# Kernel tuning notes

Measured on AMD Instinct MI355X. Metric: run time of the kernel, lower is better.

Reference implementation:

```python
import jax, jax.numpy as jnp
import numpy as np

N, D, K = 65536, 512, 512


def _l2norm(x, eps=1e-12):
    # matches torch F.normalize: x / max(||x||, eps)
    n = jnp.linalg.norm(x, axis=-1, keepdims=True)
    return x / jnp.maximum(n, eps)


def setup_inputs() -> dict:
    key = jax.random.key(0)
    k1, k2 = jax.random.split(key)
    return {
        "embeddings": jax.random.normal(k1, (N, D), dtype=jnp.float32),
        "labels": jax.random.randint(k2, (N,), 0, K),
        "w": jnp.asarray(10.0, dtype=jnp.float32),
        "b": jnp.asarray(-5.0, dtype=jnp.float32),
        "num_classes": K,
    }


def reference(embeddings, labels, w, b, num_classes):
    # assumes labels take all values in [0, num_classes) so torch.unique's
    # inverse == labels (holds for the generated inputs: 65536 draws over 512 ids)
    labels = labels.astype(jnp.int32)
    n = embeddings.shape[0]
    emb = _l2norm(embeddings)                                        # [N, D]
    ones = jnp.ones((n,), dtype=emb.dtype)
    counts = jax.ops.segment_sum(ones, labels, num_segments=num_classes)   # [K]
    sums = jax.ops.segment_sum(emb, labels, num_segments=num_classes)      # [K, D]
    centroids = sums / jnp.maximum(counts, 1.0)[:, None]             # [K, D] (NOT re-normalized, per source)
    sims = emb @ centroids.T                                          # [N, K]
    # exclusive centroid for each sample's own class, vectorized over N
    cnt_i = counts[labels]                                            # [N]
    denom = jnp.maximum(cnt_i - 1.0, 1.0)[:, None]
    excl = _l2norm((sums[labels] - emb) / denom)                      # [N, D]
    own = jnp.sum(emb * excl, axis=-1)                                # [N]
    rows = jnp.arange(n)
    cur = sims[rows, labels]
    own = jnp.where(cnt_i > 1.0, own, cur)                            # skip singleton classes
    sims = sims.at[rows, labels].set(own)
    logits = jnp.maximum(w, 1e-6) * sims + b
    logp = jax.nn.log_softmax(logits, axis=-1)
    return -jnp.mean(logp[rows, labels])
```

## Files before the change

kernel.cpp:

```cpp
#include <hip/hip_runtime.h>
#include <hip/hip_bf16.h>

#define N_ROWS 65536
#define DIM    512
#define KCLS   512
#define BUCKET 256

typedef __bf16 bf16x8 __attribute__((ext_vector_type(8)));
typedef float  f32x16 __attribute__((ext_vector_type(16)));

__device__ __forceinline__ float bf2f(ushort u) {
    union { unsigned int i; float f; } v; v.i = ((unsigned int)u) << 16; return v.f;
}

__global__ __launch_bounds__(256) void rnorm_embb_kernel(
    const float* __restrict__ emb, const int* __restrict__ labels,
    ushort* __restrict__ embb, int* __restrict__ counts,
    ushort* __restrict__ order16)
{
    const int tid  = threadIdx.x;
    const int wave = tid >> 6;
    const int lane = tid & 63;
    const int row  = blockIdx.x * 4 + wave;

    const float4* ep = (const float4*)(emb + (size_t)row * DIM + lane * 8);
    const float4 e0 = ep[0], e1 = ep[1];
    float ss = e0.x*e0.x + e0.y*e0.y + e0.z*e0.z + e0.w*e0.w
             + e1.x*e1.x + e1.y*e1.y + e1.z*e1.z + e1.w*e1.w;
    #pragma unroll
    for (int off = 1; off < 64; off <<= 1)
        ss += __shfl_xor(ss, off, 64);
    const float rn = 1.0f / fmaxf(sqrtf(ss), 1e-12f);

    bf16x8 h;
    h[0] = (__bf16)(e0.x * rn); h[1] = (__bf16)(e0.y * rn);
    h[2] = (__bf16)(e0.z * rn); h[3] = (__bf16)(e0.w * rn);
    h[4] = (__bf16)(e1.x * rn); h[5] = (__bf16)(e1.y * rn);
    h[6] = (__bf16)(e1.z * rn); h[7] = (__bf16)(e1.w * rn);
    *(bf16x8*)(embb + (size_t)row * DIM + lane * 8) = h;

    if (lane == 0) {
        const int l   = labels[row];
        const int pos = atomicAdd(&counts[l], 1);
        order16[l * BUCKET + pos] = (ushort)row;
    }
}

__global__ __launch_bounds__(256) void class_sum_kernel(
    const ushort* __restrict__ embb,
    const int* __restrict__ counts, const ushort* __restrict__ order16,
    float* __restrict__ sums, ushort* __restrict__ centb)
{
    __shared__ float part[4][DIM];

    const int cls  = blockIdx.x;
    const int tid  = threadIdx.x;
    const int wave = tid >> 6;
    const int lane = tid & 63;
    const int cnt  = counts[cls];
    const int base = cls * BUCKET;
    const int d8   = lane * 8;

    float a[8] = {};
    float b2[8] = {};
    int j = wave;
    for (; j + 4 < cnt; j += 8) {
        const int r1 = order16[base + j];
        const int r2 = order16[base + j + 4];
        const uint4 u1 = *(const uint4*)(embb + (size_t)r1 * DIM + d8);
        const uint4 u2 = *(const uint4*)(embb + (size_t)r2 * DIM + d8);
        const ushort* s1 = (const ushort*)&u1;
        const ushort* s2 = (const ushort*)&u2;
        #pragma unroll
        for (int q = 0; q < 8; ++q) { a[q] += bf2f(s1[q]); b2[q] += bf2f(s2[q]); }
    }
    if (j < cnt) {
        const int r = order16[base + j];
        const uint4 u = *(const uint4*)(embb + (size_t)r * DIM + d8);
        const ushort* s1 = (const ushort*)&u;
        #pragma unroll
        for (int q = 0; q < 8; ++q) a[q] += bf2f(s1[q]);
    }
    #pragma unroll
    for (int q = 0; q < 8; ++q) part[wave][d8 + q] = a[q] + b2[q];
    __syncthreads();

    const int d0 = tid * 2;
    const float s0 = part[0][d0]   + part[1][d0]   + part[2][d0]   + part[3][d0];
    const float s1 = part[0][d0+1] + part[1][d0+1] + part[2][d0+1] + part[3][d0+1];
    *(float2*)(sums + (size_t)cls * DIM + d0) = make_float2(s0, s1);
    const float cinv = 1.0f / fmaxf((float)cnt, 1.0f);
    const __bf16 c0 = (__bf16)(s0 * cinv);
    const __bf16 c1 = (__bf16)(s1 * cinv);
    ushort2 cpk;
    cpk.x = *(const ushort*)&c0;
    cpk.y = *(const ushort*)&c1;
    *(ushort2*)(centb + (size_t)cls * DIM + d0) = cpk;
}

#define A_STRIDE 40
#define B_STRIDE 40
__global__ __launch_bounds__(256, 3) void fused_loss_kernel(
    const ushort* __restrict__ embb, const int* __restrict__ labels,
    const int* __restrict__ counts, const float* __restrict__ sums,
    const ushort* __restrict__ centb,
    const float* __restrict__ wp, const float* __restrict__ bp,
    float* __restrict__ loss_acc, int* __restrict__ done,
    float* __restrict__ out)
{
    __shared__ __align__(16) ushort A_lds[64 * A_STRIDE];
    __shared__ __align__(16) ushort B_lds[256 * B_STRIDE];
    __shared__ float m_part[4][64];
    __shared__ float s_part[4][64];
    __shared__ float ll_s[64];
    __shared__ float own_s[64];
    __shared__ int   lbl_s[64];
    __shared__ int   rep_s[64];

    const int tid  = threadIdx.x;
    const int wave = tid >> 6;
    const int lane = tid & 63;
    const int ln31 = lane & 31;
    const int half = lane >> 5;
    const int r0   = blockIdx.x * 64;

    m_part[wave][lane] = -1e30f;
    s_part[wave][lane] = 0.f;

    for (int rr = wave; rr < 64; rr += 4) {
        const int row = r0 + rr;
        const int l   = labels[row];
        const uint4 ev = *(const uint4*)(embb + (size_t)row * DIM + lane * 8);
        const ushort* eu = (const ushort*)&ev;
        const float4* sp = (const float4*)(sums + (size_t)l * DIM + lane * 8);
        const float4 s0 = sp[0], s1 = sp[1];
        const float sv[8] = {s0.x, s0.y, s0.z, s0.w, s1.x, s1.y, s1.z, s1.w};
        float d1 = 0.f, d2 = 0.f;
        #pragma unroll
        for (int jj = 0; jj < 8; ++jj) {
            const float e  = bf2f(eu[jj]);
            const float df = sv[jj] - e;
            d1 += e * df;
            d2 += df * df;
        }
        #pragma unroll
        for (int off = 32; off > 0; off >>= 1) {
            d1 += __shfl_down(d1, off, 64);
            d2 += __shfl_down(d2, off, 64);
        }
        if (lane == 0) {
            own_s[rr] = d1 / fmaxf(sqrtf(d2), 1e-12f);
            lbl_s[rr] = l;
            rep_s[rr] = (counts[l] > 1) ? 1 : 0;
        }
    }
    __syncthreads();

    const int srow = tid >> 2;
    const int sch  = (tid & 3) * 8;
    const ushort* aSrc = embb + (size_t)(r0 + srow) * DIM + sch;
    ushort* aDst = A_lds + srow * A_STRIDE + sch;
    ushort* bDst = B_lds + srow * B_STRIDE + sch;
    const ushort* Ard = A_lds + ln31 * A_STRIDE + half * 8;
    const ushort* Brd = B_lds + (wave * 64 + ln31) * B_STRIDE + half * 8;

    const int rot = (blockIdx.x * 7) & 15;
    const float wv = fmaxf(wp[0], 1e-6f);
    const float bv = bp[0];

    #pragma unroll 1
    for (int ph = 0; ph < 2; ++ph) {
        const ushort* bBase = centb + (size_t)(ph * 256) * DIM;
        f32x16 acc[2][2] = {};

        #pragma unroll 1
        for (int ic = 0; ic < 16; ++ic) {
            const int kk = ((ic + rot) & 15) * 32;
            *(uint4*)aDst = *(const uint4*)(aSrc + kk);
            #pragma unroll
            for (int it = 0; it < 4; ++it)
                *(uint4*)(bDst + it * 64 * B_STRIDE) =
                    *(const uint4*)(bBase + (size_t)(srow + it * 64) * DIM + sch + kk);
            __syncthreads();

            #pragma unroll
            for (int ks = 0; ks < 2; ++ks) {
                const int ko = ks * 16;
                const bf16x8 a0 = *(const bf16x8*)(Ard + ko);
                const bf16x8 a1 = *(const bf16x8*)(Ard + 32 * A_STRIDE + ko);
                const bf16x8 b0 = *(const bf16x8*)(Brd + ko);
                const bf16x8 b1 = *(const bf16x8*)(Brd + 32 * B_STRIDE + ko);
                acc[0][0] = __builtin_amdgcn_mfma_f32_32x32x16_bf16(a0, b0, acc[0][0], 0, 0, 0);
                acc[0][1] = __builtin_amdgcn_mfma_f32_32x32x16_bf16(a0, b1, acc[0][1], 0, 0, 0);
                acc[1][0] = __builtin_amdgcn_mfma_f32_32x32x16_bf16(a1, b0, acc[1][0], 0, 0, 0);
                acc[1][1] = __builtin_amdgcn_mfma_f32_32x32x16_bf16(a1, b1, acc[1][1], 0, 0, 0);
            }
            __syncthreads();
        }

        #pragma unroll
        for (int mt = 0; mt < 2; ++mt) {
            #pragma unroll
            for (int reg = 0; reg < 16; ++reg) {
                const int row = mt * 32 + (reg & 3) + 8 * (reg >> 2) + 4 * half;
                const int lbl = lbl_s[row];
                float vals[2];
                float mx = -1e30f;
                #pragma unroll
                for (int jn = 0; jn < 2; ++jn) {
                    const int col = ph * 256 + wave * 64 + jn * 32 + ln31;
                    float lg = wv * acc[mt][jn][reg] + bv;
                    if (col == lbl) {
                        if (rep_s[row]) lg = wv * own_s[row] + bv;
                        ll_s[row] = lg;
                    }
                    vals[jn] = lg;
                    mx = fmaxf(mx, lg);
                }
                #pragma unroll
                for (int off = 1; off < 32; off <<= 1)
                    mx = fmaxf(mx, __shfl_xor(mx, off, 64));
                float s = __expf(vals[0] - mx) + __expf(vals[1] - mx);
                #pragma unroll
                for (int off = 1; off < 32; off <<= 1)
                    s += __shfl_xor(s, off, 64);
                if (ln31 == 0) {
                    const float mo = m_part[wave][row];
                    const float mn = fmaxf(mo, mx);
                    s_part[wave][row] = s_part[wave][row] * __expf(mo - mn)
                                      + s * __expf(mx - mn);
                    m_part[wave][row] = mn;
                }
            }
        }
    }
    __syncthreads();

    if (tid < 64) {
        const int row = tid;
        float m0 = m_part[0][row], m1 = m_part[1][row];
        float m2 = m_part[2][row], m3 = m_part[3][row];
        float mt = fmaxf(fmaxf(m0, m1), fmaxf(m2, m3));
        float st = s_part[0][row] * __expf(m0 - mt)
                 + s_part[1][row] * __expf(m1 - mt)
                 + s_part[2][row] * __expf(m2 - mt)
                 + s_part[3][row] * __expf(m3 - mt);
        float loss = mt + __logf(st) - ll_s[row];
        #pragma unroll
        for (int off = 32; off > 0; off >>= 1)
            loss += __shfl_down(loss, off, 64);
        if (tid == 0) {
            atomicAdd(loss_acc, loss);
            __threadfence();
            const int t = atomicAdd(done, 1);
            if (t == (N_ROWS / 64) - 1) {
                const float tot = atomicAdd(loss_acc, 0.0f);
                out[0] = tot / (float)N_ROWS;
            }
        }
    }
}

extern "C" void kernel_launch(void* const* d_in, const int* in_sizes, int n_in,
                              void* d_out, int out_size, void* d_ws, size_t ws_size,
                              hipStream_t stream)
{
    const float* emb    = (const float*)d_in[0];
    const int*   labels = (const int*)d_in[1];
    const float* wp     = (const float*)d_in[2];
    const float* bp     = (const float*)d_in[3];
    float* out = (float*)d_out;

    char* ws = (char*)d_ws;
    ushort* embb    = (ushort*)(ws + 0);
    ushort* order16 = (ushort*)(ws + 67108864);
    float*  sums    = (float*) (ws + 67371008);
    ushort* centb   = (ushort*)(ws + 68419584);
    int*    counts  = (int*)   (ws + 68943872);
    float*  loss_acc= (float*) (ws + 68945920);
    int*    done    = (int*)   (ws + 68945924);

    hipMemsetAsync(counts, 0, 2056, stream);

    rnorm_embb_kernel<<<N_ROWS / 4, 256, 0, stream>>>(emb, labels, embb, counts, order16);
    class_sum_kernel<<<KCLS, 256, 0, stream>>>(embb, counts, order16, sums, centb);
    fused_loss_kernel<<<N_ROWS / 64, 256, 0, stream>>>(embb, labels, counts, sums,
                                                       centb, wp, bp, loss_acc, done, out);
}
```

Baseline: 333.8 us.

## Merge three kernels into one persistent kernel with grid-wide barriers

Replaces the three separate launches (normalize/bucket, class sums, fused GEMM+loss) with a single persistent kernel of 768 blocks that uses atomic-counter grid barriers between phases. The goal is to remove launch gaps and tail effects between kernels. The GEMM phase now has uneven work per block: blocks 512 and up each process two 64-row tiles while the rest process one. Correctness relies on all 768 blocks being co-resident, which is assumed and not checked, and the spin barriers add their own latency.

New measurement: 613.5 us. 83.8% more time.

```diff
diff --git a/kernel.cpp b/kernel.cpp
--- a/kernel.cpp
+++ b/kernel.cpp
@@ -5,6 +5,7 @@
 #define DIM    512
 #define KCLS   512
 #define BUCKET 256
+#define GRID   768
 
 typedef __bf16 bf16x8 __attribute__((ext_vector_type(8)));
 typedef float  f32x16 __attribute__((ext_vector_type(16)));
@@ -13,251 +14,267 @@
     union { unsigned int i; float f; } v; v.i = ((unsigned int)u) << 16; return v.f;
 }
 
-__global__ __launch_bounds__(256) void rnorm_embb_kernel(
+#define A_STRIDE 40
+#define B_STRIDE 40
+
+#define SM_A      0
+#define SM_B      5120
+#define SM_MPART  25600
+#define SM_SPART  26624
+#define SM_LL     27648
+#define SM_OWN    27904
+#define SM_LBL    28160
+#define SM_REP    28416
+
+__global__ __launch_bounds__(256, 3) void mono_kernel(
     const float* __restrict__ emb, const int* __restrict__ labels,
-    ushort* __restrict__ embb, int* __restrict__ counts,
-    ushort* __restrict__ order16)
+    const float* __restrict__ wp, const float* __restrict__ bp,
+    ushort* __restrict__ embb, ushort* __restrict__ order16,
+    int* __restrict__ counts, float* __restrict__ sums,
+    ushort* __restrict__ centb, float* __restrict__ loss_acc,
+    int* __restrict__ bars, float* __restrict__ out)
 {
+    __shared__ __align__(16) char smem[28672];
+
     const int tid  = threadIdx.x;
     const int wave = tid >> 6;
     const int lane = tid & 63;
-    const int row  = blockIdx.x * 4 + wave;
-
-    const float4* ep = (const float4*)(emb + (size_t)row * DIM + lane * 8);
-    const float4 e0 = ep[0], e1 = ep[1];
-    float ss = e0.x*e0.x + e0.y*e0.y + e0.z*e0.z + e0.w*e0.w
-             + e1.x*e1.x + e1.y*e1.y + e1.z*e1.z + e1.w*e1.w;
-    #pragma unroll
-    for (int off = 1; off < 64; off <<= 1)
-        ss += __shfl_xor(ss, off, 64);
-    const float rn = 1.0f / fmaxf(sqrtf(ss), 1e-12f);
-
-    bf16x8 h;
-    h[0] = (__bf16)(e0.x * rn); h[1] = (__bf16)(e0.y * rn);
-    h[2] = (__bf16)(e0.z * rn); h[3] = (__bf16)(e0.w * rn);
-    h[4] = (__bf16)(e1.x * rn); h[5] = (__bf16)(e1.y * rn);
-    h[6] = (__bf16)(e1.z * rn); h[7] = (__bf16)(e1.w * rn);
-    *(bf16x8*)(embb + (size_t)row * DIM + lane * 8) = h;
-
-    if (lane == 0) {
-        const int l   = labels[row];
-        const int pos = atomicAdd(&counts[l], 1);
-        order16[l * BUCKET + pos] = (ushort)row;
+    const int bid  = blockIdx.x;
+
+    auto grid_barrier = [&](int* bar) {
+        __syncthreads();
+        if (tid == 0) {
+            __threadfence();
+            atomicAdd(bar, 1);
+            while (atomicAdd(bar, 0) < GRID) __builtin_amdgcn_s_sleep(1);
+            __threadfence();
+        }
+        __syncthreads();
+    };
+
+    for (int c = bid; c < N_ROWS / 4; c += GRID) {
+        const int row = c * 4 + wave;
+        const float4* ep = (const float4*)(emb + (size_t)row * DIM + lane * 8);
+        const float4 e0 = ep[0], e1 = ep[1];
+        float ss = e0.x*e0.x + e0.y*e0.y + e0.z*e0.z + e0.w*e0.w
+                 + e1.x*e1.x + e1.y*e1.y + e1.z*e1.z + e1.w*e1.w;
+        #pragma unroll
+        for (int off = 1; off < 64; off <<= 1)
+            ss += __shfl_xor(ss, off, 64);
+        const float rn = 1.0f / fmaxf(sqrtf(ss), 1e-12f);
+
+        bf16x8 h;
+        h[0] = (__bf16)(e0.x * rn); h[1] = (__bf16)(e0.y * rn);
+        h[2] = (__bf16)(e0.z * rn); h[3] = (__bf16)(e0.w * rn);
+        h[4] = (__bf16)(e1.x * rn); h[5] = (__bf16)(e1.y * rn);
+        h[6] = (__bf16)(e1.z * rn); h[7] = (__bf16)(e1.w * rn);
+        *(bf16x8*)(embb + (size_t)row * DIM + lane * 8) = h;
+
+        if (lane == 0) {
+            const int l   = labels[row];
+            const int pos = atomicAdd(&counts[l], 1);
+            order16[l * BUCKET + pos] = (ushort)row;
+        }
     }
-}
-
-__global__ __launch_bounds__(256) void class_sum_kernel(
-    const ushort* __restrict__ embb,
-    const int* __restrict__ counts, const ushort* __restrict__ order16,
-    float* __restrict__ sums, ushort* __restrict__ centb)
-{
-    __shared__ float part[4][DIM];
-
-    const int cls  = blockIdx.x;
-    const int tid  = threadIdx.x;
-    const int wave = tid >> 6;
-    const int lane = tid & 63;
-    const int cnt  = counts[cls];
-    const int base = cls * BUCKET;
-    const int d8   = lane * 8;
-
-    float a[8] = {};
-    float b2[8] = {};
-    int j = wave;
-    for (; j + 4 < cnt; j += 8) {
-        const int r1 = order16[base + j];
-        const int r2 = order16[base + j + 4];
-        const uint4 u1 = *(const uint4*)(embb + (size_t)r1 * DIM + d8);
-        const uint4 u2 = *(const uint4*)(embb + (size_t)r2 * DIM + d8);
-        const ushort* s1 = (const ushort*)&u1;
-        const ushort* s2 = (const ushort*)&u2;
+    grid_barrier(&bars[0]);
+
+    if (bid < KCLS) {
+        float* part = (float*)smem;
+        const int cls  = bid;
+        const int cnt  = counts[cls];
+        const int base = cls * BUCKET;
+        const int d8   = lane * 8;
+
+        float a[8] = {};
+        float b2[8] = {};
+        int j = wave;
+        for (; j + 4 < cnt; j += 8) {
+            const int r1 = order16[base + j];
+            const int r2 = order16[base + j + 4];
+            const uint4 u1 = *(const uint4*)(embb + (size_t)r1 * DIM + d8);
+            const uint4 u2 = *(const uint4*)(embb + (size_t)r2 * DIM + d8);
+            const ushort* s1 = (const ushort*)&u1;
+            const ushort* s2 = (const ushort*)&u2;
+            #pragma unroll
+            for (int q = 0; q < 8; ++q) { a[q] += bf2f(s1[q]); b2[q] += bf2f(s2[q]); }
+        }
+        if (j < cnt) {
+            const int r = order16[base + j];
+            const uint4 u = *(const uint4*)(embb + (size_t)r * DIM + d8);
+            const ushort* s1 = (const ushort*)&u;
+            #pragma unroll
+            for (int q = 0; q < 8; ++q) a[q] += bf2f(s1[q]);
+        }
         #pragma unroll
-        for (int q = 0; q < 8; ++q) { a[q] += bf2f(s1[q]); b2[q] += bf2f(s2[q]); }
+        for (int q = 0; q < 8; ++q) part[wave * DIM + d8 + q] = a[q] + b2[q];
+        __syncthreads();
+
+        const int d0 = tid * 2;
+        const float s0 = part[0*DIM+d0]   + part[1*DIM+d0]   + part[2*DIM+d0]   + part[3*DIM+d0];
+        const float s1 = part[0*DIM+d0+1] + part[1*DIM+d0+1] + part[2*DIM+d0+1] + part[3*DIM+d0+1];
+        *(float2*)(sums + (size_t)cls * DIM + d0) = make_float2(s0, s1);
+        const float cinv = 1.0f / fmaxf((float)cnt, 1.0f);
+        const __bf16 c0 = (__bf16)(s0 * cinv);
+        const __bf16 c1 = (__bf16)(s1 * cinv);
+        ushort2 cpk;
+        cpk.x = *(const ushort*)&c0;
+        cpk.y = *(const ushort*)&c1;
+        *(ushort2*)(centb + (size_t)cls * DIM + d0) = cpk;
     }
-    if (j < cnt) {
-        const int r = order16[base + j];
-        const uint4 u = *(const uint4*)(embb + (size_t)r * DIM + d8);
-        const ushort* s1 = (const ushort*)&u;
-        #pragma unroll
-        for (int q = 0; q < 8; ++q) a[q] += bf2f(s1[q]);
-    }
-    #pragma unroll
-    for (int q = 0; q < 8; ++q) part[wave][d8 + q] = a[q] + b2[q];
-    __syncthreads();
-
-    const int d0 = tid * 2;
-    const float s0 = part[0][d0]   + part[1][d0]   + part[2][d0]   + part[3][d0];
-    const float s1 = part[0][d0+1] + part[1][d0+1] + part[2][d0+1] + part[3][d0+1];
-    *(float2*)(sums + (size_t)cls * DIM + d0) = make_float2(s0, s1);
-    const float cinv = 1.0f / fmaxf((float)cnt, 1.0f);
-    const __bf16 c0 = (__bf16)(s0 * cinv);
-    const __bf16 c1 = (__bf16)(s1 * cinv);
-    ushort2 cpk;
-    cpk.x = *(const ushort*)&c0;
-    cpk.y = *(const ushort*)&c1;
-    *(ushort2*)(centb + (size_t)cls * DIM + d0) = cpk;
-}
-
-#define A_STRIDE 40
-#define B_STRIDE 40
-__global__ __launch_bounds__(256, 3) void fused_loss_kernel(
-    const ushort* __restrict__ embb, const int* __restrict__ labels,
-    const int* __restrict__ counts, const float* __restrict__ sums,
-    const ushort* __restrict__ centb,
-    const float* __restrict__ wp, const float* __restrict__ bp,
-    float* __restrict__ loss_acc, int* __restrict__ done,
-    float* __restrict__ out)
-{
-    __shared__ __align__(16) ushort A_lds[64 * A_STRIDE];
-    __shared__ __align__(16) ushort B_lds[256 * B_STRIDE];
-    __shared__ float m_part[4][64];
-    __shared__ float s_part[4][64];
-    __shared__ float ll_s[64];
-    __shared__ float own_s[64];
-    __shared__ int   lbl_s[64];
-    __shared__ int   rep_s[64];
-
-    const int tid  = threadIdx.x;
-    const int wave = tid >> 6;
-    const int lane = tid & 63;
+    grid_barrier(&bars[1]);
+
+    ushort* A_lds = (ushort*)(smem + SM_A);
+    ushort* B_lds = (ushort*)(smem + SM_B);
+    float*  m_part = (float*)(smem + SM_MPART);
+    float*  s_part = (float*)(smem + SM_SPART);
+    float*  ll_s   = (float*)(smem + SM_LL);
+    float*  own_s  = (float*)(smem + SM_OWN);
+    int*    lbl_s  = (int*)  (smem + SM_LBL);
+    int*    rep_s  = (int*)  (smem + SM_REP);
+
     const int ln31 = lane & 31;
     const int half = lane >> 5;
-    const int r0   = blockIdx.x * 64;
-
-    m_part[wave][lane] = -1e30f;
-    s_part[wave][lane] = 0.f;
-
-    for (int rr = wave; rr < 64; rr += 4) {
-        const int row = r0 + rr;
-        const int l   = labels[row];
-        const uint4 ev = *(const uint4*)(embb + (size_t)row * DIM + lane * 8);
-        const ushort* eu = (const ushort*)&ev;
-        const float4* sp = (const float4*)(sums + (size_t)l * DIM + lane * 8);
-        const float4 s0 = sp[0], s1 = sp[1];
-        const float sv[8] = {s0.x, s0.y, s0.z, s0.w, s1.x, s1.y, s1.z, s1.w};
-        float d1 = 0.f, d2 = 0.f;
-        #pragma unroll
-        for (int jj = 0; jj < 8; ++jj) {
-            const float e  = bf2f(eu[jj]);
-            const float df = sv[jj] - e;
-            d1 += e * df;
-            d2 += df * df;
-        }
-        #pragma unroll
-        for (int off = 32; off > 0; off >>= 1) {
-            d1 += __shfl_down(d1, off, 64);
-            d2 += __shfl_down(d2, off, 64);
-        }
-        if (lane == 0) {
-            own_s[rr] = d1 / fmaxf(sqrtf(d2), 1e-12f);
-            lbl_s[rr] = l;
-            rep_s[rr] = (counts[l] > 1) ? 1 : 0;
-        }
-    }
-    __syncthreads();
-
     const int srow = tid >> 2;
     const int sch  = (tid & 3) * 8;
-    const ushort* aSrc = embb + (size_t)(r0 + srow) * DIM + sch;
-    ushort* aDst = A_lds + srow * A_STRIDE + sch;
-    ushort* bDst = B_lds + srow * B_STRIDE + sch;
-    const ushort* Ard = A_lds + ln31 * A_STRIDE + half * 8;
-    const ushort* Brd = B_lds + (wave * 64 + ln31) * B_STRIDE + half * 8;
-
-    const int rot = (blockIdx.x * 7) & 15;
     const float wv = fmaxf(wp[0], 1e-6f);
     const float bv = bp[0];
 
     #pragma unroll 1
-    for (int ph = 0; ph < 2; ++ph) {
-        const ushort* bBase = centb + (size_t)(ph * 256) * DIM;
-        f32x16 acc[2][2] = {};
+    for (int rep = 0; rep < 2; ++rep) {
+        if (rep == 1 && bid < 512) break;
+        const int t  = (rep == 0) ? bid : bid + 256;
+        const int r0 = t * 64;
+
+        __syncthreads();
+        m_part[wave * 64 + lane] = -1e30f;
+        s_part[wave * 64 + lane] = 0.f;
+
+        for (int rr = wave; rr < 64; rr += 4) {
+            const int row = r0 + rr;
+            const int l   = labels[row];
+            const uint4 ev = *(const uint4*)(embb + (size_t)row * DIM + lane * 8);
+            const ushort* eu = (const ushort*)&ev;
+            const float4* sp = (const float4*)(sums + (size_t)l * DIM + lane * 8);
+            const float4 s0 = sp[0], s1 = sp[1];
+            const float sv[8] = {s0.x, s0.y, s0.z, s0.w, s1.x, s1.y, s1.z, s1.w};
+            float d1 = 0.f, d2 = 0.f;
+            #pragma unroll
+            for (int jj = 0; jj < 8; ++jj) {
+                const float e  = bf2f(eu[jj]);
+                const float df = sv[jj] - e;
+                d1 += e * df;
+                d2 += df * df;
+            }
+            #pragma unroll
+            for (int off = 32; off > 0; off >>= 1) {
+                d1 += __shfl_down(d1, off, 64);
+                d2 += __shfl_down(d2, off, 64);
+            }
+            if (lane == 0) {
+                own_s[rr] = d1 / fmaxf(sqrtf(d2), 1e-12f);
+                lbl_s[rr] = l;
+                rep_s[rr] = (counts[l] > 1) ? 1 : 0;
+            }
+        }
+        __syncthreads();
+
+        const ushort* aSrc = embb + (size_t)(r0 + srow) * DIM + sch;
+        ushort* aDst = A_lds + srow * A_STRIDE + sch;
+        ushort* bDst = B_lds + srow * B_STRIDE + sch;
+        const ushort* Ard = A_lds + ln31 * A_STRIDE + half * 8;
+        const ushort* Brd = B_lds + (wave * 64 + ln31) * B_STRIDE + half * 8;
+        const int rot = (t * 7) & 15;
 
         #pragma unroll 1
-        for (int ic = 0; ic < 16; ++ic) {
-            const int kk = ((ic + rot) & 15) * 32;
-            *(uint4*)aDst = *(const uint4*)(aSrc + kk);
-            #pragma unroll
-            for (int it = 0; it < 4; ++it)
-                *(uint4*)(bDst + it * 64 * B_STRIDE) =
-                    *(const uint4*)(bBase + (size_t)(srow + it * 64) * DIM + sch + kk);
-            __syncthreads();
-
-            #pragma unroll
-            for (int ks = 0; ks < 2; ++ks) {
-                const int ko = ks * 16;
-                const bf16x8 a0 = *(const bf16x8*)(Ard + ko);
-                const bf16x8 a1 = *(const bf16x8*)(Ard + 32 * A_STRIDE + ko);
-                const bf16x8 b0 = *(const bf16x8*)(Brd + ko);
-                const bf16x8 b1 = *(const bf16x8*)(Brd + 32 * B_STRIDE + ko);
-                acc[0][0] = __builtin_amdgcn_mfma_f32_32x32x16_bf16(a0, b0, acc[0][0], 0, 0, 0);
-                acc[0][1] = __builtin_amdgcn_mfma_f32_32x32x16_bf16(a0, b1, acc[0][1], 0, 0, 0);
-                acc[1][0] = __builtin_amdgcn_mfma_f32_32x32x16_bf16(a1, b0, acc[1][0], 0, 0, 0);
-                acc[1][1] = __builtin_amdgcn_mfma_f32_32x32x16_bf16(a1, b1, acc[1][1], 0, 0, 0);
-            }
-            __syncthreads();
-        }
-
-        #pragma unroll
-        for (int mt = 0; mt < 2; ++mt) {
-            #pragma unroll
-            for (int reg = 0; reg < 16; ++reg) {
-                const int row = mt * 32 + (reg & 3) + 8 * (reg >> 2) + 4 * half;
-                const int lbl = lbl_s[row];
-                float vals[2];
-                float mx = -1e30f;
+        for (int ph = 0; ph < 2; ++ph) {
+            const ushort* bBase = centb + (size_t)(ph * 256) * DIM;
+            f32x16 acc[2][2] = {};
+
+            #pragma unroll 1
+            for (int ic = 0; ic < 16; ++ic) {
+                const int kk = ((ic + rot) & 15) * 32;
+                *(uint4*)aDst = *(const uint4*)(aSrc + kk);
                 #pragma unroll
-                for (int jn = 0; jn < 2; ++jn) {
-                    const int col = ph * 256 + wave * 64 + jn * 32 + ln31;
-                    float lg = wv * acc[mt][jn][reg] + bv;
-                    if (col == lbl) {
-                        if (rep_s[row]) lg = wv * own_s[row] + bv;
-                        ll_s[row] = lg;
+                for (int it = 0; it < 4; ++it)
+                    *(uint4*)(bDst + it * 64 * B_STRIDE) =
+                        *(const uint4*)(bBase + (size_t)(srow + it * 64) * DIM + sch + kk);
+                __syncthreads();
+
+                #pragma unroll
+                for (int ks = 0; ks < 2; ++ks) {
+                    const int ko = ks * 16;
+                    const bf16x8 a0 = *(const bf16x8*)(Ard + ko);
+                    const bf16x8 a1 = *(const bf16x8*)(Ard + 32 * A_STRIDE + ko);
+                    const bf16x8 b0 = *(const bf16x8*)(Brd + ko);
+                    const bf16x8 b1 = *(const bf16x8*)(Brd + 32 * B_STRIDE + ko);
+                    acc[0][0] = __builtin_amdgcn_mfma_f32_32x32x16_bf16(a0, b0, acc[0][0], 0, 0, 0);
+                    acc[0][1] = __builtin_amdgcn_mfma_f32_32x32x16_bf16(a0, b1, acc[0][1], 0, 0, 0);
+                    acc[1][0] = __builtin_amdgcn_mfma_f32_32x32x16_bf16(a1, b0, acc[1][0], 0, 0, 0);
+                    acc[1][1] = __builtin_amdgcn_mfma_f32_32x32x16_bf16(a1, b1, acc[1][1], 0, 0, 0);
+                }
+                __syncthreads();
+            }
+
+            #pragma unroll
+            for (int mt = 0; mt < 2; ++mt) {
+                #pragma unroll
+                for (int reg = 0; reg < 16; ++reg) {
+                    const int row = mt * 32 + (reg & 3) + 8 * (reg >> 2) + 4 * half;
+                    const int lbl = lbl_s[row];
+                    float vals[2];
+                    float mx = -1e30f;
+                    #pragma unroll
+                    for (int jn = 0; jn < 2; ++jn) {
+                        const int col = ph * 256 + wave * 64 + jn * 32 + ln31;
+                        float lg = wv * acc[mt][jn][reg] + bv;
+                        if (col == lbl) {
+                            if (rep_s[row]) lg = wv * own_s[row] + bv;
+                            ll_s[row] = lg;
+                        }
+                        vals[jn] = lg;
+                        mx = fmaxf(mx, lg);
                     }
-                    vals[jn] = lg;
-                    mx = fmaxf(mx, lg);
+                    #pragma unroll
+                    for (int off = 1; off < 32; off <<= 1)
+                        mx = fmaxf(mx, __shfl_xor(mx, off, 64));
+                    float s = __expf(vals[0] - mx) + __expf(vals[1] - mx);
+                    #pragma unroll
+                    for (int off = 1; off < 32; off <<= 1)
+                        s += __shfl_xor(s, off, 64);
+                    if (ln31 == 0) {
+                        const float mo = m_part[wave * 64 + row];
+                        const float mn = fmaxf(mo, mx);
+                        s_part[wave * 64 + row] = s_part[wave * 64 + row] * __expf(mo - mn)
+                                                + s * __expf(mx - mn);
+                        m_part[wave * 64 + row] = mn;
+                    }
                 }
-                #pragma unroll
-                for (int off = 1; off < 32; off <<= 1)
-                    mx = fmaxf(mx, __shfl_xor(mx, off, 64));
-                float s = __expf(vals[0] - mx) + __expf(vals[1] - mx);
-                #pragma unroll
-                for (int off = 1; off < 32; off <<= 1)
-                    s += __shfl_xor(s, off, 64);
-                if (ln31 == 0) {
-                    const float mo = m_part[wave][row];
-                    const float mn = fmaxf(mo, mx);
-                    s_part[wave][row] = s_part[wave][row] * __expf(mo - mn)
-                                      + s * __expf(mx - mn);
-                    m_part[wave][row] = mn;
-                }
-            }
-        }
+            }
+        }
+        __syncthreads();
+
+        if (tid < 64) {
+            const int row = tid;
+            float m0 = m_part[0*64+row], m1 = m_part[1*64+row];
+            float m2 = m_part[2*64+row], m3 = m_part[3*64+row];
+            float mt = fmaxf(fmaxf(m0, m1), fmaxf(m2, m3));
+            float st = s_part[0*64+row] * __expf(m0 - mt)
+                     + s_part[1*64+row] * __expf(m1 - mt)
+                     + s_part[2*64+row] * __expf(m2 - mt)
+                     + s_part[3*64+row] * __expf(m3 - mt);
+            float loss = mt + __logf(st) - ll_s[row];
+            #pragma unroll
+            for (int off = 32; off > 0; off >>= 1)
+                loss += __shfl_down(loss, off, 64);
+            if (tid == 0) atomicAdd(loss_acc, loss);
+        }
+        __syncthreads();
     }
-    __syncthreads();
-
-    if (tid < 64) {
-        const int row = tid;
-        float m0 = m_part[0][row], m1 = m_part[1][row];
-        float m2 = m_part[2][row], m3 = m_part[3][row];
-        float mt = fmaxf(fmaxf(m0, m1), fmaxf(m2, m3));
-        float st = s_part[0][row] * __expf(m0 - mt)
-                 + s_part[1][row] * __expf(m1 - mt)
-                 + s_part[2][row] * __expf(m2 - mt)
-                 + s_part[3][row] * __expf(m3 - mt);
-        float loss = mt + __logf(st) - ll_s[row];
-        #pragma unroll
-        for (int off = 32; off > 0; off >>= 1)
-            loss += __shfl_down(loss, off, 64);
-        if (tid == 0) {
-            atomicAdd(loss_acc, loss);
-            __threadfence();
-            const int t = atomicAdd(done, 1);
-            if (t == (N_ROWS / 64) - 1) {
-                const float tot = atomicAdd(loss_acc, 0.0f);
-                out[0] = tot / (float)N_ROWS;
-            }
-        }
+
+    grid_barrier(&bars[2]);
+    if (bid == 0 && tid == 0) {
+        const float tot = atomicAdd(loss_acc, 0.0f);
+        out[0] = tot / (float)N_ROWS;
     }
 }
 
@@ -278,12 +295,10 @@
     ushort* centb   = (ushort*)(ws + 68419584);
     int*    counts  = (int*)   (ws + 68943872);
     float*  loss_acc= (float*) (ws + 68945920);
-    int*    done    = (int*)   (ws + 68945924);
-
-    hipMemsetAsync(counts, 0, 2056, stream);
-
-    rnorm_embb_kernel<<<N_ROWS / 4, 256, 0, stream>>>(emb, labels, embb, counts, order16);
-    class_sum_kernel<<<KCLS, 256, 0, stream>>>(embb, counts, order16, sums, centb);
-    fused_loss_kernel<<<N_ROWS / 64, 256, 0, stream>>>(embb, labels, counts, sums,
-                                                       centb, wp, bp, loss_acc, done, out);
+    int*    bars    = (int*)   (ws + 68945924);
+
+    hipMemsetAsync(counts, 0, 2064, stream);
+
+    mono_kernel<<<GRID, 256, 0, stream>>>(emb, labels, wp, bp, embb, order16,
+                                          counts, sums, centb, loss_acc, bars, out);
 }
```
